# Performance work log

Hardware: AMD Instinct MI355X
Metric: run time of the kernel (lower is better)

The kernel has to match this reference:

```python
import jax, jax.numpy as jnp
import numpy as np

N_NODES = 100000
N_EDGES = 1600000
IN_DIM = 256
OUT_DIM = 64


def setup_inputs() -> dict:
    key = jax.random.key(0)
    k1, k2, k3, k4, k5 = jax.random.split(key, 5)
    x = jax.random.normal(k1, (N_NODES, IN_DIM), dtype=jnp.float32)
    # glorot init as in weight_variable_glorot
    limit = np.sqrt(6.0 / (IN_DIM + OUT_DIM))
    weight = jax.random.uniform(k2, (IN_DIM, OUT_DIM), dtype=jnp.float32,
                                minval=-limit, maxval=limit)
    edge_src = jax.random.randint(k3, (N_EDGES,), 0, N_NODES, dtype=jnp.int32)
    edge_dst = jax.random.randint(k4, (N_EDGES,), 0, N_NODES, dtype=jnp.int32)
    edge_w = jax.random.uniform(k5, (N_EDGES,), dtype=jnp.float32)
    return {"x": x, "weight": weight, "edge_src": edge_src,
            "edge_dst": edge_dst, "edge_w": edge_w}


def reference(x, weight, edge_src, edge_dst, edge_w):
    # dense mm: [N, in] @ [in, out] -> [N, out]
    xw = x @ weight
    # spmm with COO adjacency: out[dst] += w * xw[src]
    msgs = xw[edge_src] * edge_w[:, None]          # [E, out]
    agg = jax.ops.segment_sum(msgs, edge_dst, num_segments=N_NODES)
    # activation (default act = ReLU)
    return jax.nn.relu(agg)
```

## Files before the change

kernel.cpp:

```cpp
#include <hip/hip_runtime.h>

constexpr int IN_DIM  = 256;
constexpr int OUT_DIM = 64;
constexpr int NPB     = 64;
constexpr int NBK     = 2048;
constexpr int CAPB    = 1280;

typedef __attribute__((ext_vector_type(8))) _Float16 f16x8;
typedef __attribute__((ext_vector_type(4))) float f32x4;

__device__ __forceinline__ void gload_lds16(const void* g, void* l) {
    __builtin_amdgcn_global_load_lds(
        (const __attribute__((address_space(1))) void*)g,
        (__attribute__((address_space(3))) void*)l, 16, 0, 0);
}

__global__ __launch_bounds__(64) void wfrag_k(const float* __restrict__ W,
                                              f16x8* __restrict__ frag,
                                              int* __restrict__ cnt) {
    const int gid = blockIdx.x * 64 + threadIdx.x;
    cnt[gid] = 0;

    const int kt = blockIdx.x >> 2;
    const int nt = blockIdx.x & 3;
    const int l  = threadIdx.x;
    const int col = nt * 16 + (l & 15);
    const int k0  = kt * 32 + (l >> 4) * 8;
    f16x8 h;
#pragma unroll
    for (int j = 0; j < 8; ++j)
        h[j] = (_Float16)W[(size_t)(k0 + j) * OUT_DIM + col];
    frag[blockIdx.x * 64 + l] = h;
}

__global__ __launch_bounds__(256, 4) void gemm_part_k(
        const float* __restrict__ x,
        const f16x8* __restrict__ frag,
        unsigned short* __restrict__ xw,
        const int* __restrict__ esrc, const int* __restrict__ edst,
        const float* __restrict__ ew,
        int* __restrict__ cnt, int2* __restrict__ rec,
        int N, int E, int GB, int NB) {
    __shared__ char smem[32768];
    const int bid = blockIdx.x;
    const int tid = threadIdx.x;

    if (bid >= GB) {
        int* h  = (int*)smem;
        int* bb = (int*)smem + NBK;
        for (int i = tid; i < NBK; i += 256) h[i] = 0;
        __syncthreads();

        const int e0 = (bid - GB) * 4096;
        int sv[16];
        float wv[16];
        int br[16];
#pragma unroll
        for (int q = 0; q < 4; ++q) {
            const int eb = e0 + (q * 256 + tid) * 4;
            if (eb + 3 < E) {
                int4  d4 = *reinterpret_cast<const int4*>(edst + eb);
                int4  s4 = *reinterpret_cast<const int4*>(esrc + eb);
                float4 w4 = *reinterpret_cast<const float4*>(ew + eb);
                int d[4] = {d4.x, d4.y, d4.z, d4.w};
                sv[q * 4 + 0] = s4.x; sv[q * 4 + 1] = s4.y;
                sv[q * 4 + 2] = s4.z; sv[q * 4 + 3] = s4.w;
                wv[q * 4 + 0] = w4.x; wv[q * 4 + 1] = w4.y;
                wv[q * 4 + 2] = w4.z; wv[q * 4 + 3] = w4.w;
#pragma unroll
                for (int j = 0; j < 4; ++j) {
                    int b = d[j] >> 6;
                    int r = atomicAdd(&h[b], 1);
                    br[q * 4 + j] = (b << 18) | ((d[j] & 63) << 12) | r;
                }
            } else {
#pragma unroll
                for (int j = 0; j < 4; ++j) {
                    int e = eb + j;
                    br[q * 4 + j] = -1;
                    if (e < E) {
                        int d = edst[e];
                        sv[q * 4 + j] = esrc[e];
                        wv[q * 4 + j] = ew[e];
                        int b = d >> 6;
                        int r = atomicAdd(&h[b], 1);
                        br[q * 4 + j] = (b << 18) | ((d & 63) << 12) | r;
                    }
                }
            }
        }
        __syncthreads();
        for (int i = tid; i < NB; i += 256) {
            int c = h[i];
            bb[i] = c ? atomicAdd(&cnt[i], c) : 0;
        }
        __syncthreads();
#pragma unroll
        for (int j = 0; j < 16; ++j) {
            if (br[j] >= 0) {
                int b = br[j] >> 18;
                int dlow = (br[j] >> 12) & 63;
                int slot = bb[b] + (br[j] & 0xFFF);
                if (slot < CAPB)
                    rec[(size_t)b * CAPB + slot] =
                        make_int2(sv[j] | (dlow << 17), __float_as_int(wv[j]));
            }
        }
        return;
    }

    const int lane = tid & 63;
    const int wid  = tid >> 6;
    const int row0 = bid * 128;
    const int rlo = lane & 15, khi = lane >> 4;

    f16x8 FR[8];
#pragma unroll
    for (int kt = 0; kt < 8; ++kt)
        FR[kt] = frag[(kt * 4 + wid) * 64 + lane];

    float* buf0 = (float*)smem;
    float* buf1 = (float*)(smem + 16384);

    auto STAGE = [&](float* buf, int tile) {
#pragma unroll
        for (int i = 0; i < 4; ++i) {
            int rit = i * 4 + wid;
            int gr = row0 + tile * 16 + rit;
            if (gr > N - 1) gr = N - 1;
            int slot = lane ^ (rit & 7);
            gload_lds16(x + (size_t)gr * IN_DIM + slot * 4,
                        (char*)buf + rit * 1024);
        }
    };

    STAGE(buf0, 0);
    __syncthreads();

    const int sw = (rlo & 7) << 4;

    for (int t = 0; t < 8; ++t) {
        float* cur = (t & 1) ? buf1 : buf0;
        float* nxt = (t & 1) ? buf0 : buf1;
        if (t < 7) STAGE(nxt, t + 1);

        const char* xrow = (const char*)cur + rlo * 1024;
        f32x4 acc = (f32x4){0.f, 0.f, 0.f, 0.f};
#pragma unroll
        for (int kt = 0; kt < 8; ++kt) {
            const int L0 = kt * 128 + khi * 32;
            float4 a0 = *reinterpret_cast<const float4*>(xrow + (L0 ^ sw));
            float4 a1 = *reinterpret_cast<const float4*>(xrow + ((L0 + 16) ^ sw));
            f16x8 ah;
            ah[0] = (_Float16)a0.x;
            ah[1] = (_Float16)a0.y;
            ah[2] = (_Float16)a0.z;
            ah[3] = (_Float16)a0.w;
            ah[4] = (_Float16)a1.x;
            ah[5] = (_Float16)a1.y;
            ah[6] = (_Float16)a1.z;
            ah[7] = (_Float16)a1.w;
            acc = __builtin_amdgcn_mfma_f32_16x16x32_f16(ah, FR[kt], acc, 0, 0, 0);
        }
#pragma unroll
        for (int i = 0; i < 4; ++i) {
            int row = row0 + t * 16 + khi * 4 + i;
            if (row < N) {
                unsigned u = __float_as_uint(acc[i]);
                u += 0x7fffu + ((u >> 16) & 1u);
                xw[(size_t)row * OUT_DIM + wid * 16 + rlo] =
                    (unsigned short)(u >> 16);
            }
        }
        __syncthreads();
    }
}

__global__ __launch_bounds__(256) void fingather_k(
        const unsigned short* __restrict__ xw,
        const int2* __restrict__ rec, const int* __restrict__ cnt,
        float* __restrict__ out, int N) {
    __shared__ int cnt_s[NPB];
    __shared__ int sc[NPB];
    __shared__ int cur_s[NPB];
    __shared__ int off_s[NPB + 1];
    __shared__ int2 val_s[CAPB];
    const int t = threadIdx.x;
    const int b = blockIdx.x;
    const size_t s = (size_t)b * CAPB;
    const int sz = min(cnt[b], CAPB);

    if (t < NPB) cnt_s[t] = 0;
    __syncthreads();
    for (int i = t; i < sz; i += 256)
        atomicAdd(&cnt_s[(rec[s + i].x >> 17) & 63], 1);
    __syncthreads();

    if (t < NPB) sc[t] = cnt_s[t];
    __syncthreads();
#pragma unroll
    for (int o = 1; o < NPB; o <<= 1) {
        int a = 0;
        if (t < NPB && t >= o) a = sc[t - o];
        __syncthreads();
        if (t < NPB) sc[t] += a;
        __syncthreads();
    }
    if (t < NPB) {
        cur_s[t] = sc[t] - cnt_s[t];
        off_s[t + 1] = sc[t];
    }
    if (t == 0) off_s[0] = 0;
    __syncthreads();

    for (int i = t; i < sz; i += 256) {
        int2 r = rec[s + i];
        int slot = atomicAdd(&cur_s[(r.x >> 17) & 63], 1);
        val_s[slot] = make_int2(r.x & 0x1FFFF, r.y);
    }
    __syncthreads();

    const int lane = t & 63, wid = t >> 6;
    const int g = lane >> 3, sl = lane & 7;

    for (int n = wid; n < NPB; n += 4) {
        const int node = b * NPB + n;
        if (node >= N) break;
        const int b0 = off_s[n], e0 = off_s[n + 1];
        float acc[8];
#pragma unroll
        for (int j = 0; j < 8; ++j) acc[j] = 0.f;

        for (int i = b0; i < e0; i += 32) {
            int idx0 = i + g;
            int idx1 = i + g + 8;
            int idx2 = i + g + 16;
            int idx3 = i + g + 24;
            int2 r0 = val_s[min(idx0, e0 - 1)];
            int2 r1 = val_s[min(idx1, e0 - 1)];
            int2 r2 = val_s[min(idx2, e0 - 1)];
            int2 r3 = val_s[min(idx3, e0 - 1)];
            float w0 = (idx0 < e0) ? __int_as_float(r0.y) : 0.f;
            float w1 = (idx1 < e0) ? __int_as_float(r1.y) : 0.f;
            float w2 = (idx2 < e0) ? __int_as_float(r2.y) : 0.f;
            float w3 = (idx3 < e0) ? __int_as_float(r3.y) : 0.f;
            int4 q0 = *reinterpret_cast<const int4*>(
                xw + (size_t)r0.x * OUT_DIM + sl * 8);
            int4 q1 = *reinterpret_cast<const int4*>(
                xw + (size_t)r1.x * OUT_DIM + sl * 8);
            int4 q2 = *reinterpret_cast<const int4*>(
                xw + (size_t)r2.x * OUT_DIM + sl * 8);
            int4 q3 = *reinterpret_cast<const int4*>(
                xw + (size_t)r3.x * OUT_DIM + sl * 8);
#define ACCUM(Q, W)                                                   \
            {                                                         \
                unsigned u0 = (unsigned)Q.x, u1 = (unsigned)Q.y;      \
                unsigned u2 = (unsigned)Q.z, u3 = (unsigned)Q.w;      \
                acc[0] += W * __uint_as_float(u0 << 16);              \
                acc[1] += W * __uint_as_float(u0 & 0xFFFF0000u);      \
                acc[2] += W * __uint_as_float(u1 << 16);              \
                acc[3] += W * __uint_as_float(u1 & 0xFFFF0000u);      \
                acc[4] += W * __uint_as_float(u2 << 16);              \
                acc[5] += W * __uint_as_float(u2 & 0xFFFF0000u);      \
                acc[6] += W * __uint_as_float(u3 << 16);              \
                acc[7] += W * __uint_as_float(u3 & 0xFFFF0000u);      \
            }
            ACCUM(q0, w0)
            ACCUM(q1, w1)
            ACCUM(q2, w2)
            ACCUM(q3, w3)
#undef ACCUM
        }

#pragma unroll
        for (int m = 8; m < 64; m <<= 1)
#pragma unroll
            for (int j = 0; j < 8; ++j)
                acc[j] += __shfl_xor(acc[j], m);

        if (g == 0) {
            float4 v0 = make_float4(fmaxf(acc[0], 0.f), fmaxf(acc[1], 0.f),
                                    fmaxf(acc[2], 0.f), fmaxf(acc[3], 0.f));
            float4 v1 = make_float4(fmaxf(acc[4], 0.f), fmaxf(acc[5], 0.f),
                                    fmaxf(acc[6], 0.f), fmaxf(acc[7], 0.f));
            float4* op = reinterpret_cast<float4*>(
                out + (size_t)node * OUT_DIM + sl * 8);
            op[0] = v0;
            op[1] = v1;
        }
    }
}

extern "C" void kernel_launch(void* const* d_in, const int* in_sizes, int n_in,
                              void* d_out, int out_size, void* d_ws, size_t ws_size,
                              hipStream_t stream) {
    const float* x    = (const float*)d_in[0];
    const float* W    = (const float*)d_in[1];
    const int*   esrc = (const int*)d_in[2];
    const int*   edst = (const int*)d_in[3];
    const float* ew   = (const float*)d_in[4];
    float* out = (float*)d_out;

    const int N  = in_sizes[0] / IN_DIM;
    const int E  = in_sizes[2];
    const int NB = (N + NPB - 1) / NPB;
    const int GB = (N + 127) / 128;
    const int PB = (E + 4095) / 4096;

    char* ws = (char*)d_ws;
    size_t o = 0;
    f16x8* frag = (f16x8*)(ws + o);     o += 32 * 64 * 16;
    unsigned short* xw = (unsigned short*)(ws + o);
    o += (size_t)N * OUT_DIM * 2;
    int2* rec = (int2*)(ws + o);        o += (size_t)NB * CAPB * 8;
    int* cnt  = (int*)(ws + o);         o += NBK * 4;

    wfrag_k<<<32, 64, 0, stream>>>(W, frag, cnt);
    gemm_part_k<<<GB + PB, 256, 0, stream>>>(x, frag, xw,
                                             esrc, edst, ew, cnt, rec,
                                             N, E, GB, NB);
    fingather_k<<<NB, 256, 0, stream>>>(xw, rec, cnt, out, N);
}
```

Measured before the change: 89.39 us.

## Use 1024-thread blocks for fused GEMM and edge-partition kernel

Grows the fused GEMM/partition blocks from 256 to 1024 threads. GEMM blocks now cover 512 rows, with 16 waves splitting into 4 row sub-tiles by 4 column tiles over a single 64 KB LDS stage, replacing the previous double buffer. Partition blocks spread the same 4096 edges over 1024 threads at 4 edges per thread, which lowers register use. The aim is fewer, larger blocks and more parallelism per edge chunk, at the cost of losing load/compute overlap in the GEMM and limiting blocks per CU because of the larger LDS footprint.

```diff
diff --git a/kernel.cpp b/kernel.cpp
--- a/kernel.cpp
+++ b/kernel.cpp
@@ -33,7 +33,7 @@
     frag[blockIdx.x * 64 + l] = h;
 }
 
-__global__ __launch_bounds__(256, 4) void gemm_part_k(
+__global__ __launch_bounds__(1024, 8) void gemm_part_k(
         const float* __restrict__ x,
         const f16x8* __restrict__ frag,
         unsigned short* __restrict__ xw,
@@ -41,66 +41,60 @@
         const float* __restrict__ ew,
         int* __restrict__ cnt, int2* __restrict__ rec,
         int N, int E, int GB, int NB) {
-    __shared__ char smem[32768];
+    __shared__ char smem[65536];
     const int bid = blockIdx.x;
     const int tid = threadIdx.x;
 
     if (bid >= GB) {
         int* h  = (int*)smem;
         int* bb = (int*)smem + NBK;
-        for (int i = tid; i < NBK; i += 256) h[i] = 0;
-        __syncthreads();
-
-        const int e0 = (bid - GB) * 4096;
-        int sv[16];
-        float wv[16];
-        int br[16];
-#pragma unroll
-        for (int q = 0; q < 4; ++q) {
-            const int eb = e0 + (q * 256 + tid) * 4;
-            if (eb + 3 < E) {
-                int4  d4 = *reinterpret_cast<const int4*>(edst + eb);
-                int4  s4 = *reinterpret_cast<const int4*>(esrc + eb);
-                float4 w4 = *reinterpret_cast<const float4*>(ew + eb);
-                int d[4] = {d4.x, d4.y, d4.z, d4.w};
-                sv[q * 4 + 0] = s4.x; sv[q * 4 + 1] = s4.y;
-                sv[q * 4 + 2] = s4.z; sv[q * 4 + 3] = s4.w;
-                wv[q * 4 + 0] = w4.x; wv[q * 4 + 1] = w4.y;
-                wv[q * 4 + 2] = w4.z; wv[q * 4 + 3] = w4.w;
-#pragma unroll
-                for (int j = 0; j < 4; ++j) {
-                    int b = d[j] >> 6;
+        for (int i = tid; i < NBK; i += 1024) h[i] = 0;
+        __syncthreads();
+
+        const int e0 = (bid - GB) * 4096 + tid * 4;
+        int sv[4];
+        float wv[4];
+        int br4[4];
+        if (e0 + 3 < E) {
+            int4  d4 = *reinterpret_cast<const int4*>(edst + e0);
+            int4  s4 = *reinterpret_cast<const int4*>(esrc + e0);
+            float4 w4 = *reinterpret_cast<const float4*>(ew + e0);
+            sv[0] = s4.x; sv[1] = s4.y; sv[2] = s4.z; sv[3] = s4.w;
+            wv[0] = w4.x; wv[1] = w4.y; wv[2] = w4.z; wv[3] = w4.w;
+            int d[4] = {d4.x, d4.y, d4.z, d4.w};
+#pragma unroll
+            for (int j = 0; j < 4; ++j) {
+                int b = d[j] >> 6;
+                int r = atomicAdd(&h[b], 1);
+                br4[j] = (b << 18) | ((d[j] & 63) << 12) | r;
+            }
+        } else {
+#pragma unroll
+            for (int j = 0; j < 4; ++j) {
+                int e = e0 + j;
+                br4[j] = -1;
+                if (e < E) {
+                    int d = edst[e];
+                    sv[j] = esrc[e];
+                    wv[j] = ew[e];
+                    int b = d >> 6;
                     int r = atomicAdd(&h[b], 1);
-                    br[q * 4 + j] = (b << 18) | ((d[j] & 63) << 12) | r;
+                    br4[j] = (b << 18) | ((d & 63) << 12) | r;
                 }
-            } else {
-#pragma unroll
-                for (int j = 0; j < 4; ++j) {
-                    int e = eb + j;
-                    br[q * 4 + j] = -1;
-                    if (e < E) {
-                        int d = edst[e];
-                        sv[q * 4 + j] = esrc[e];
-                        wv[q * 4 + j] = ew[e];
-                        int b = d >> 6;
-                        int r = atomicAdd(&h[b], 1);
-                        br[q * 4 + j] = (b << 18) | ((d & 63) << 12) | r;
-                    }
-                }
-            }
-        }
-        __syncthreads();
-        for (int i = tid; i < NB; i += 256) {
+            }
+        }
+        __syncthreads();
+        for (int i = tid; i < NB; i += 1024) {
             int c = h[i];
             bb[i] = c ? atomicAdd(&cnt[i], c) : 0;
         }
         __syncthreads();
 #pragma unroll
-        for (int j = 0; j < 16; ++j) {
-            if (br[j] >= 0) {
-                int b = br[j] >> 18;
-                int dlow = (br[j] >> 12) & 63;
-                int slot = bb[b] + (br[j] & 0xFFF);
+        for (int j = 0; j < 4; ++j) {
+            if (br4[j] >= 0) {
+                int b = br4[j] >> 18;
+                int dlow = (br4[j] >> 12) & 63;
+                int slot = bb[b] + (br4[j] & 0xFFF);
                 if (slot < CAPB)
                     rec[(size_t)b * CAPB + slot] =
                         make_int2(sv[j] | (dlow << 17), __float_as_int(wv[j]));
@@ -110,41 +104,33 @@
     }
 
     const int lane = tid & 63;
-    const int wid  = tid >> 6;
-    const int row0 = bid * 128;
+    const int w    = tid >> 6;
+    const int sub  = w >> 2;
+    const int nt   = w & 3;
+    const int row0 = bid * 512;
     const int rlo = lane & 15, khi = lane >> 4;
 
     f16x8 FR[8];
 #pragma unroll
     for (int kt = 0; kt < 8; ++kt)
-        FR[kt] = frag[(kt * 4 + wid) * 64 + lane];
-
-    float* buf0 = (float*)smem;
-    float* buf1 = (float*)(smem + 16384);
-
-    auto STAGE = [&](float* buf, int tile) {
+        FR[kt] = frag[(kt * 4 + nt) * 64 + lane];
+
+    float* buf = (float*)smem;
+    const int sw = (rlo & 7) << 4;
+
+    for (int t = 0; t < 8; ++t) {
 #pragma unroll
         for (int i = 0; i < 4; ++i) {
-            int rit = i * 4 + wid;
-            int gr = row0 + tile * 16 + rit;
+            int r = i * 16 + w;
+            int gr = row0 + t * 64 + r;
             if (gr > N - 1) gr = N - 1;
-            int slot = lane ^ (rit & 7);
+            int slot = lane ^ (r & 7);
             gload_lds16(x + (size_t)gr * IN_DIM + slot * 4,
-                        (char*)buf + rit * 1024);
-        }
-    };
-
-    STAGE(buf0, 0);
-    __syncthreads();
-
-    const int sw = (rlo & 7) << 4;
-
-    for (int t = 0; t < 8; ++t) {
-        float* cur = (t & 1) ? buf1 : buf0;
-        float* nxt = (t & 1) ? buf0 : buf1;
-        if (t < 7) STAGE(nxt, t + 1);
-
-        const char* xrow = (const char*)cur + rlo * 1024;
+                        (char*)buf + r * 1024);
+        }
+        __syncthreads();
+
+        const char* xrow = (const char*)buf + (sub * 16 + rlo) * 1024;
         f32x4 acc = (f32x4){0.f, 0.f, 0.f, 0.f};
 #pragma unroll
         for (int kt = 0; kt < 8; ++kt) {
@@ -164,11 +150,11 @@
         }
 #pragma unroll
         for (int i = 0; i < 4; ++i) {
-            int row = row0 + t * 16 + khi * 4 + i;
+            int row = row0 + t * 64 + sub * 16 + khi * 4 + i;
             if (row < N) {
                 unsigned u = __float_as_uint(acc[i]);
                 u += 0x7fffu + ((u >> 16) & 1u);
-                xw[(size_t)row * OUT_DIM + wid * 16 + rlo] =
+                xw[(size_t)row * OUT_DIM + nt * 16 + rlo] =
                     (unsigned short)(u >> 16);
             }
         }
@@ -304,7 +290,7 @@
     const int N  = in_sizes[0] / IN_DIM;
     const int E  = in_sizes[2];
     const int NB = (N + NPB - 1) / NPB;
-    const int GB = (N + 127) / 128;
+    const int GB = (N + 511) / 512;
     const int PB = (E + 4095) / 4096;
 
     char* ws = (char*)d_ws;
@@ -316,8 +302,8 @@
     int* cnt  = (int*)(ws + o);         o += NBK * 4;
 
     wfrag_k<<<32, 64, 0, stream>>>(W, frag, cnt);
-    gemm_part_k<<<GB + PB, 256, 0, stream>>>(x, frag, xw,
-                                             esrc, edst, ew, cnt, rec,
-                                             N, E, GB, NB);
+    gemm_part_k<<<GB + PB, 1024, 0, stream>>>(x, frag, xw,
+                                              esrc, edst, ew, cnt, rec,
+                                              N, E, GB, NB);
     fingather_k<<<NB, 256, 0, stream>>>(xw, rec, cnt, out, N);
 }
```

Result: slower. 96.03 us (+7.4%).
